# Optimization experiments

Measured on AMD Instinct MI355X. Metric: run time of the kernel, lower is better.

The kernel has to match this reference:

```python
import jax, jax.numpy as jnp
import numpy as np

S, B, E, H = 2048, 2, 1024, 16
D = E // H  # head dim = 64


def setup_inputs() -> dict:
    key = jax.random.key(0)
    k1, k2, k3 = jax.random.split(key, 3)
    x = jax.random.normal(k1, (S, B, E), dtype=jnp.float32)
    Wqkv = jax.random.normal(k2, (3 * E, E), dtype=jnp.float32) * (E ** -0.5)
    bqkv = jax.random.normal(k3, (3 * E,), dtype=jnp.float32) * 0.02
    return {"x": x, "Wqkv": Wqkv, "bqkv": bqkv}


def reference(x, Wqkv, bqkv):
    s, b, e = x.shape
    h, d = H, E // H
    # fused QKV projection: [S,B,E] @ [E,3E] -> [S,B,3E]
    qkv = jnp.einsum('sbe,fe->sbf', x, Wqkv) + bqkv
    q, k, v = jnp.split(qkv, 3, axis=-1)
    q = q.reshape(s, b, h, d)
    k = k.reshape(s, b, h, d)
    v = v.reshape(s, b, h, d)
    scale = 1.0 / jnp.sqrt(jnp.asarray(d, dtype=x.dtype))
    # scores: [B,H,S,S]
    scores = jnp.einsum('sbhd,tbhd->bhst', q, k) * scale
    attn = jax.nn.softmax(scores, axis=-1)
    # context: [S,B,H,D] -> [S,B,E]
    ctx = jnp.einsum('bhst,tbhd->sbhd', attn, v)
    return ctx.reshape(s, b, e)
```

## Files before the change

kernel.cpp:

```cpp
#include <hip/hip_runtime.h>

constexpr int SEQ   = 2048;
constexpr int BATCH = 2;
constexpr int EMB   = 1024;
constexpr int NH    = 16;
constexpr int HDIM  = 64;
constexpr int MROWS = SEQ * BATCH;
constexpr int KDIM  = EMB;
constexpr int NCOLS = 3 * EMB;

typedef __bf16 bf16x8 __attribute__((ext_vector_type(8)));
typedef __bf16 bf16x4 __attribute__((ext_vector_type(4)));
typedef float  f32x4  __attribute__((ext_vector_type(4)));
typedef float  f32x16 __attribute__((ext_vector_type(16)));
typedef unsigned int u32;
typedef unsigned int u32x4 __attribute__((ext_vector_type(4)));

__device__ __forceinline__ u32 cvt_pk_bf16(float lo, float hi) {
  u32 r;
  asm("v_cvt_pk_bf16_f32 %0, %1, %2" : "=v"(r) : "v"(lo), "v"(hi));
  return r;
}
__device__ __forceinline__ void pl32_swap(u32& a, u32& b) {
  asm("v_permlane32_swap_b32 %0, %1" : "+v"(a), "+v"(b));
}
__device__ __forceinline__ void g2l16(const __bf16* g, __bf16* l) {
  __builtin_amdgcn_global_load_lds(
      (const __attribute__((address_space(1))) void*)g,
      (__attribute__((address_space(3))) void*)l, 16, 0, 0);
}

__global__ __launch_bounds__(256) void cvt_f32_bf16(
    const float* __restrict__ src, __bf16* __restrict__ dst, int n4) {
  int stride = gridDim.x * blockDim.x;
  for (int i = blockIdx.x * blockDim.x + threadIdx.x; i < n4; i += stride) {
    float4 v = reinterpret_cast<const float4*>(src)[i];
    bf16x4 o;
    o[0] = (__bf16)v.x; o[1] = (__bf16)v.y; o[2] = (__bf16)v.z; o[3] = (__bf16)v.w;
    reinterpret_cast<bf16x4*>(dst)[i] = o;
  }
}

__global__ __launch_bounds__(256, 4) void qkv_gemm(
    const __bf16* __restrict__ Xb, const __bf16* __restrict__ Wb,
    const float* __restrict__ bqkv,
    __bf16* __restrict__ Qb, __bf16* __restrict__ Kb, __bf16* __restrict__ Vt) {
  __shared__ __attribute__((aligned(16))) __bf16 Al[2][128 * 32];
  __shared__ __attribute__((aligned(16))) __bf16 Bl[2][128 * 32];

  const int tid  = threadIdx.x;
  const int lane = tid & 63;
  const int w    = tid >> 6;
  const int wm   = w >> 1, wn = w & 1;

  const int bid  = blockIdx.x;
  const int wgid = (bid & 7) * 96 + (bid >> 3);
  const int nx   = wgid % 24;
  const int nyy  = wgid / 24;
  const int m0   = nyy * 128;
  const int n0   = nx * 128;

  f32x4 acc[4][4] = {};

  auto stage = [&](int buf, int kt) {
#pragma unroll
    for (int c = 0; c < 2; ++c) {
      const int u   = (w * 2 + c) * 64 + lane;
      const int row = u >> 2;
      const int sc  = ((u & 3) ^ ((row >> 1) & 3)) * 8;
      g2l16(&Xb[(size_t)(m0 + row) * KDIM + kt * 32 + sc], &Al[buf][(w * 2 + c) * 512]);
      g2l16(&Wb[(size_t)(n0 + row) * KDIM + kt * 32 + sc], &Bl[buf][(w * 2 + c) * 512]);
    }
  };

  stage(0, 0);
  __syncthreads();

  const int l15 = lane & 15, hi4 = lane >> 4;
  const int cswz = (hi4 ^ ((l15 >> 1) & 3)) * 8;

  for (int kt = 0; kt < KDIM / 32; ++kt) {
    const int buf = kt & 1;
    if (kt + 1 < KDIM / 32) stage(buf ^ 1, kt + 1);

    bf16x8 af[4], bfr[4];
#pragma unroll
    for (int i = 0; i < 4; ++i) {
      af[i]  = *reinterpret_cast<const bf16x8*>(&Al[buf][(wm * 64 + i * 16 + l15) * 32 + cswz]);
      bfr[i] = *reinterpret_cast<const bf16x8*>(&Bl[buf][(wn * 64 + i * 16 + l15) * 32 + cswz]);
    }
    __builtin_amdgcn_s_setprio(1);
#pragma unroll
    for (int i = 0; i < 4; ++i)
#pragma unroll
      for (int j = 0; j < 4; ++j)
        acc[i][j] = __builtin_amdgcn_mfma_f32_16x16x32_bf16(af[i], bfr[j], acc[i][j], 0, 0, 0);
    __builtin_amdgcn_s_setprio(0);
    __syncthreads();
  }

  const float QSCALE = 0.18033688011112042f;
#pragma unroll
  for (int j = 0; j < 4; ++j) {
    const int f    = n0 + wn * 64 + j * 16 + l15;
    const float bias = bqkv[f];
    const int sec  = f >> 10;
    const int hd   = f & 1023;
    const int h    = hd >> 6, d = hd & 63;
#pragma unroll
    for (int i = 0; i < 4; ++i) {
#pragma unroll
      for (int r = 0; r < 4; ++r) {
        const int mm = m0 + wm * 64 + i * 16 + hi4 * 4 + r;
        const int s_ = mm >> 1, b_ = mm & 1;
        const int bh = b_ * NH + h;
        const float val = acc[i][j][r] + bias;
        if (sec == 0) {
          Qb[((size_t)bh * SEQ + s_) * HDIM + d] = (__bf16)(val * QSCALE);
        } else if (sec == 1) {
          Kb[((size_t)bh * SEQ + s_) * HDIM + d] = (__bf16)val;
        } else {
          Vt[((size_t)bh * HDIM + d) * SEQ + s_] = (__bf16)val;
        }
      }
    }
  }
}

__global__ __launch_bounds__(128, 4) void attn_fwd(
    const __bf16* __restrict__ Qb, const __bf16* __restrict__ Kb,
    const __bf16* __restrict__ Vt, float* __restrict__ out) {
  __shared__ __attribute__((aligned(16))) __bf16 lds[16384];

  const int tid  = threadIdx.x;
  const int lane = tid & 63;
  const int w    = tid >> 6;
  const int lq   = lane & 31;
  const int hi   = lane >> 5;

  const int bid  = blockIdx.x;
  const int wgid = (bid & 7) * 128 + (bid >> 3);
  const int qi   = wgid & 31;
  const int bh   = wgid >> 5;
  const int b_   = bh >> 4, h = bh & 15;
  const int q0   = qi * 64 + w * 32;

  const __bf16* Qp = Qb + (size_t)bh * SEQ * HDIM;
  const __bf16* Kp = Kb + (size_t)bh * SEQ * HDIM;
  const __bf16* Vp = Vt + (size_t)bh * HDIM * SEQ;

  bf16x8 qf[4];
#pragma unroll
  for (int ks = 0; ks < 4; ++ks)
    qf[ks] = *reinterpret_cast<const bf16x8*>(&Qp[(size_t)(q0 + lq) * HDIM + ks * 16 + hi * 8]);

  f32x16 acc0 = {}, acc1 = {};
  float m = -1e30f, l = 0.f;

  auto stage = [&](int b, int t0) {
#pragma unroll
    for (int c = 0; c < 4; ++c) {
      const int u   = (w * 4 + c) * 64 + lane;
      const int row = u >> 3;
      const int sc  = ((u & 7) * 8) ^ ((row & 7) << 3);
      g2l16(Kp + (size_t)(t0 + row) * HDIM + sc, lds + b * 8192 + (w * 4 + c) * 512);
      g2l16(Vp + (size_t)row * SEQ + t0 + sc,    lds + b * 8192 + 4096 + (w * 4 + c) * 512);
    }
  };

  stage(0, 0);
  __syncthreads();

  for (int t0 = 0; t0 < SEQ; t0 += 64) {
    const int cur = (t0 >> 6) & 1;
    if (t0 + 64 < SEQ) stage(cur ^ 1, t0 + 64);
    const __bf16* kb = lds + cur * 8192;
    const __bf16* vb = kb + 4096;

    f32x16 S0 = {}, S1 = {};
    __builtin_amdgcn_s_setprio(1);
#pragma unroll
    for (int ks = 0; ks < 4; ++ks) {
      const int colb = ks * 16 + hi * 8;
      bf16x8 k0 = *reinterpret_cast<const bf16x8*>(&kb[lq * 64        + (colb ^ ((lq & 7) << 3))]);
      bf16x8 k1 = *reinterpret_cast<const bf16x8*>(&kb[(32 + lq) * 64 + (colb ^ ((lq & 7) << 3))]);
      S0 = __builtin_amdgcn_mfma_f32_32x32x16_bf16(k0, qf[ks], S0, 0, 0, 0);
      S1 = __builtin_amdgcn_mfma_f32_32x32x16_bf16(k1, qf[ks], S1, 0, 0, 0);
    }
    __builtin_amdgcn_s_setprio(0);

    float pmax;
    {
      float t0m = fmaxf(S0[0], S0[1]), t1m = fmaxf(S0[2], S0[3]);
      float t2m = fmaxf(S0[4], S0[5]), t3m = fmaxf(S0[6], S0[7]);
      float t4m = fmaxf(S0[8], S0[9]), t5m = fmaxf(S0[10], S0[11]);
      float t6m = fmaxf(S0[12], S0[13]), t7m = fmaxf(S0[14], S0[15]);
      t0m = fmaxf(t0m, t1m); t2m = fmaxf(t2m, t3m); t4m = fmaxf(t4m, t5m); t6m = fmaxf(t6m, t7m);
      float a_ = fmaxf(fmaxf(t0m, t2m), fmaxf(t4m, t6m));
      float u0 = fmaxf(S1[0], S1[1]), u1 = fmaxf(S1[2], S1[3]);
      float u2 = fmaxf(S1[4], S1[5]), u3 = fmaxf(S1[6], S1[7]);
      float u4 = fmaxf(S1[8], S1[9]), u5 = fmaxf(S1[10], S1[11]);
      float u6 = fmaxf(S1[12], S1[13]), u7 = fmaxf(S1[14], S1[15]);
      u0 = fmaxf(u0, u1); u2 = fmaxf(u2, u3); u4 = fmaxf(u4, u5); u6 = fmaxf(u6, u7);
      float b2 = fmaxf(fmaxf(u0, u2), fmaxf(u4, u6));
      pmax = fmaxf(a_, b2);
    }
    pmax = fmaxf(pmax, __shfl_xor(pmax, 32));

    if (__any(pmax > m + 8.f)) {
      const float mnew  = fmaxf(m, pmax);
      const float alpha = __builtin_amdgcn_exp2f(m - mnew);
      m = mnew;
      l *= alpha;
#pragma unroll
      for (int i = 0; i < 16; ++i) { acc0[i] *= alpha; acc1[i] *= alpha; }
    }

    float r0 = 0.f, r1 = 0.f, r2 = 0.f, r3 = 0.f;
#pragma unroll
    for (int i = 0; i < 4; ++i) {
      S0[i]      = __builtin_amdgcn_exp2f(S0[i] - m);      r0 += S0[i];
      S0[i + 4]  = __builtin_amdgcn_exp2f(S0[i + 4] - m);  r1 += S0[i + 4];
      S0[i + 8]  = __builtin_amdgcn_exp2f(S0[i + 8] - m);  r2 += S0[i + 8];
      S0[i + 12] = __builtin_amdgcn_exp2f(S0[i + 12] - m); r3 += S0[i + 12];
    }
#pragma unroll
    for (int i = 0; i < 4; ++i) {
      S1[i]      = __builtin_amdgcn_exp2f(S1[i] - m);      r0 += S1[i];
      S1[i + 4]  = __builtin_amdgcn_exp2f(S1[i + 4] - m);  r1 += S1[i + 4];
      S1[i + 8]  = __builtin_amdgcn_exp2f(S1[i + 8] - m);  r2 += S1[i + 8];
      S1[i + 12] = __builtin_amdgcn_exp2f(S1[i + 12] - m); r3 += S1[i + 12];
    }
    l += (r0 + r1) + (r2 + r3);

    bf16x8 pw[4];
    {
      auto mk = [&](const f32x16& P, bf16x8* dst) {
#pragma unroll
        for (int kk = 0; kk < 2; ++kk) {
          u32 a0 = cvt_pk_bf16(P[kk * 8 + 0], P[kk * 8 + 1]);
          u32 b0 = cvt_pk_bf16(P[kk * 8 + 4], P[kk * 8 + 5]);
          u32 a1 = cvt_pk_bf16(P[kk * 8 + 2], P[kk * 8 + 3]);
          u32 b1 = cvt_pk_bf16(P[kk * 8 + 6], P[kk * 8 + 7]);
          pl32_swap(a0, b0);
          pl32_swap(a1, b1);
          u32x4 wv; wv[0] = a0; wv[1] = a1; wv[2] = b0; wv[3] = b1;
          dst[kk] = __builtin_bit_cast(bf16x8, wv);
        }
      };
      mk(S0, &pw[0]);
      mk(S1, &pw[2]);
    }

    __builtin_amdgcn_s_setprio(1);
#pragma unroll
    for (int ks = 0; ks < 4; ++ks) {
      const int colb = ks * 16 + hi * 8;
      bf16x8 v0 = *reinterpret_cast<const bf16x8*>(&vb[lq * 64        + (colb ^ ((lq & 7) << 3))]);
      bf16x8 v1 = *reinterpret_cast<const bf16x8*>(&vb[(32 + lq) * 64 + (colb ^ ((lq & 7) << 3))]);
      acc0 = __builtin_amdgcn_mfma_f32_32x32x16_bf16(v0, pw[ks], acc0, 0, 0, 0);
      acc1 = __builtin_amdgcn_mfma_f32_32x32x16_bf16(v1, pw[ks], acc1, 0, 0, 0);
    }
    __builtin_amdgcn_s_setprio(0);

    __syncthreads();
  }

  l += __shfl_xor(l, 32);
  const float inv = 1.0f / l;
  const int s_ = q0 + lq;
  float* op = out + ((size_t)s_ * BATCH + b_) * EMB + h * HDIM;
#pragma unroll
  for (int rr = 0; rr < 4; ++rr) {
    float4 o0 = {acc0[4 * rr] * inv, acc0[4 * rr + 1] * inv,
                 acc0[4 * rr + 2] * inv, acc0[4 * rr + 3] * inv};
    *reinterpret_cast<float4*>(&op[8 * rr + 4 * hi]) = o0;
    float4 o1 = {acc1[4 * rr] * inv, acc1[4 * rr + 1] * inv,
                 acc1[4 * rr + 2] * inv, acc1[4 * rr + 3] * inv};
    *reinterpret_cast<float4*>(&op[8 * rr + 4 * hi + 32]) = o1;
  }
}

extern "C" void kernel_launch(void* const* d_in, const int* in_sizes, int n_in,
                              void* d_out, int out_size, void* d_ws, size_t ws_size,
                              hipStream_t stream) {
  (void)in_sizes; (void)n_in; (void)out_size; (void)ws_size;
  const float* x    = (const float*)d_in[0];
  const float* Wqkv = (const float*)d_in[1];
  const float* bias = (const float*)d_in[2];
  float* out = (float*)d_out;

  char* ws = (char*)d_ws;
  __bf16* Xb = (__bf16*)(ws);
  __bf16* Wb = (__bf16*)(ws + 8388608);
  __bf16* Qb = (__bf16*)(ws + 14680064);
  __bf16* Kb = (__bf16*)(ws + 23068672);
  __bf16* Vt = (__bf16*)(ws + 31457280);

  cvt_f32_bf16<<<dim3(1024), dim3(256), 0, stream>>>(x, Xb, (MROWS * KDIM) / 4);
  cvt_f32_bf16<<<dim3(768), dim3(256), 0, stream>>>(Wqkv, Wb, (NCOLS * KDIM) / 4);
  qkv_gemm<<<dim3(768), dim3(256), 0, stream>>>(Xb, Wb, bias, Qb, Kb, Vt);
  attn_fwd<<<dim3(1024), dim3(128), 0, stream>>>(Qb, Kb, Vt, out);
}
```

Baseline: 115.4 us.

## Split attention over key halves with combine kernel; merge conversion launches

Attention is split into two halves of the key sequence (flash-decoding style), doubling the workgroup count to 2048. Each half writes unnormalized partial outputs plus max/sum to workspace, and a new combine kernel merges them. The two fp32-to-bf16 conversion launches are also merged into one. This adds roughly 32 MB of extra partial-output traffic, one more kernel launch, and a dependence on workspace size, with a fallback to the single-pass path when the workspace is too small.

```diff
diff --git a/kernel.cpp b/kernel.cpp
--- a/kernel.cpp
+++ b/kernel.cpp
@@ -30,14 +30,19 @@
       (__attribute__((address_space(3))) void*)l, 16, 0, 0);
 }
 
-__global__ __launch_bounds__(256) void cvt_f32_bf16(
-    const float* __restrict__ src, __bf16* __restrict__ dst, int n4) {
+constexpr int N4X = (MROWS * KDIM) / 4;
+constexpr int N4W = (NCOLS * KDIM) / 4;
+__global__ __launch_bounds__(256) void cvt_all(
+    const float* __restrict__ x, const float* __restrict__ Wq,
+    __bf16* __restrict__ Xb, __bf16* __restrict__ Wb) {
   int stride = gridDim.x * blockDim.x;
-  for (int i = blockIdx.x * blockDim.x + threadIdx.x; i < n4; i += stride) {
-    float4 v = reinterpret_cast<const float4*>(src)[i];
+  for (int i = blockIdx.x * blockDim.x + threadIdx.x; i < N4X + N4W; i += stride) {
+    const float4 v = (i < N4X) ? reinterpret_cast<const float4*>(x)[i]
+                               : reinterpret_cast<const float4*>(Wq)[i - N4X];
     bf16x4 o;
     o[0] = (__bf16)v.x; o[1] = (__bf16)v.y; o[2] = (__bf16)v.z; o[3] = (__bf16)v.w;
-    reinterpret_cast<bf16x4*>(dst)[i] = o;
+    if (i < N4X) reinterpret_cast<bf16x4*>(Xb)[i] = o;
+    else         reinterpret_cast<bf16x4*>(Wb)[i - N4X] = o;
   }
 }
 
@@ -127,9 +132,11 @@
   }
 }
 
+template <int SPLIT>
 __global__ __launch_bounds__(128, 4) void attn_fwd(
     const __bf16* __restrict__ Qb, const __bf16* __restrict__ Kb,
-    const __bf16* __restrict__ Vt, float* __restrict__ out) {
+    const __bf16* __restrict__ Vt, float* __restrict__ out,
+    float* __restrict__ Op, float2* __restrict__ ml) {
   __shared__ __attribute__((aligned(16))) __bf16 lds[16384];
 
   const int tid  = threadIdx.x;
@@ -138,12 +145,19 @@
   const int lq   = lane & 31;
   const int hi   = lane >> 5;
 
-  const int bid  = blockIdx.x;
-  const int wgid = (bid & 7) * 128 + (bid >> 3);
-  const int qi   = wgid & 31;
-  const int bh   = wgid >> 5;
-  const int b_   = bh >> 4, h = bh & 15;
-  const int q0   = qi * 64 + w * 32;
+  const int bid = blockIdx.x;
+  int bh, qi, half, t_begin, nt;
+  if constexpr (SPLIT) {
+    const int wgid = (bid & 7) * 256 + (bid >> 3);
+    bh = wgid >> 6; qi = (wgid >> 1) & 31; half = wgid & 1;
+    t_begin = half * (SEQ / 2); nt = SEQ / 128;
+  } else {
+    const int wgid = (bid & 7) * 128 + (bid >> 3);
+    bh = wgid >> 5; qi = wgid & 31; half = 0;
+    t_begin = 0; nt = SEQ / 64;
+  }
+  const int b_ = bh >> 4, h = bh & 15;
+  const int q0 = qi * 64 + w * 32;
 
   const __bf16* Qp = Qb + (size_t)bh * SEQ * HDIM;
   const __bf16* Kp = Kb + (size_t)bh * SEQ * HDIM;
@@ -168,12 +182,12 @@
     }
   };
 
-  stage(0, 0);
+  stage(0, t_begin);
   __syncthreads();
 
-  for (int t0 = 0; t0 < SEQ; t0 += 64) {
-    const int cur = (t0 >> 6) & 1;
-    if (t0 + 64 < SEQ) stage(cur ^ 1, t0 + 64);
+  for (int it = 0; it < nt; ++it) {
+    const int cur = it & 1;
+    if (it + 1 < nt) stage(cur ^ 1, t_begin + (it + 1) * 64);
     const __bf16* kb = lds + cur * 8192;
     const __bf16* vb = kb + 4096;
 
@@ -267,24 +281,58 @@
   }
 
   l += __shfl_xor(l, 32);
-  const float inv = 1.0f / l;
-  const int s_ = q0 + lq;
-  float* op = out + ((size_t)s_ * BATCH + b_) * EMB + h * HDIM;
-#pragma unroll
-  for (int rr = 0; rr < 4; ++rr) {
-    float4 o0 = {acc0[4 * rr] * inv, acc0[4 * rr + 1] * inv,
-                 acc0[4 * rr + 2] * inv, acc0[4 * rr + 3] * inv};
-    *reinterpret_cast<float4*>(&op[8 * rr + 4 * hi]) = o0;
-    float4 o1 = {acc1[4 * rr] * inv, acc1[4 * rr + 1] * inv,
-                 acc1[4 * rr + 2] * inv, acc1[4 * rr + 3] * inv};
-    *reinterpret_cast<float4*>(&op[8 * rr + 4 * hi + 32]) = o1;
-  }
+  if constexpr (SPLIT) {
+    const int rowg = (bh * 32 + qi) * 64 + w * 32 + lq;
+    float* pp = Op + ((size_t)rowg * 2 + half) * 64;
+#pragma unroll
+    for (int rr = 0; rr < 4; ++rr) {
+      float4 o0 = {acc0[4 * rr], acc0[4 * rr + 1], acc0[4 * rr + 2], acc0[4 * rr + 3]};
+      *reinterpret_cast<float4*>(&pp[8 * rr + 4 * hi]) = o0;
+      float4 o1 = {acc1[4 * rr], acc1[4 * rr + 1], acc1[4 * rr + 2], acc1[4 * rr + 3]};
+      *reinterpret_cast<float4*>(&pp[8 * rr + 4 * hi + 32]) = o1;
+    }
+    if (hi == 0) ml[rowg * 2 + half] = make_float2(m, l);
+  } else {
+    const float inv = 1.0f / l;
+    const int s_ = q0 + lq;
+    float* op = out + ((size_t)s_ * BATCH + b_) * EMB + h * HDIM;
+#pragma unroll
+    for (int rr = 0; rr < 4; ++rr) {
+      float4 o0 = {acc0[4 * rr] * inv, acc0[4 * rr + 1] * inv,
+                   acc0[4 * rr + 2] * inv, acc0[4 * rr + 3] * inv};
+      *reinterpret_cast<float4*>(&op[8 * rr + 4 * hi]) = o0;
+      float4 o1 = {acc1[4 * rr] * inv, acc1[4 * rr + 1] * inv,
+                   acc1[4 * rr + 2] * inv, acc1[4 * rr + 3] * inv};
+      *reinterpret_cast<float4*>(&op[8 * rr + 4 * hi + 32]) = o1;
+    }
+  }
+}
+
+__global__ __launch_bounds__(256) void attn_combine(
+    const float* __restrict__ Op, const float2* __restrict__ ml,
+    float* __restrict__ out) {
+  const int idx  = blockIdx.x * 256 + threadIdx.x;
+  const int rowg = idx >> 4;
+  const int c    = idx & 15;
+  const float2 a = ml[rowg * 2];
+  const float2 b = ml[rowg * 2 + 1];
+  const float M  = fmaxf(a.x, b.x);
+  const float w0 = __builtin_amdgcn_exp2f(a.x - M);
+  const float w1 = __builtin_amdgcn_exp2f(b.x - M);
+  const float inv = 1.0f / (a.y * w0 + b.y * w1);
+  const float4 o0 = *reinterpret_cast<const float4*>(&Op[((size_t)rowg * 2) * 64 + c * 4]);
+  const float4 o1 = *reinterpret_cast<const float4*>(&Op[((size_t)rowg * 2 + 1) * 64 + c * 4]);
+  float4 o = {(o0.x * w0 + o1.x * w1) * inv, (o0.y * w0 + o1.y * w1) * inv,
+              (o0.z * w0 + o1.z * w1) * inv, (o0.w * w0 + o1.w * w1) * inv};
+  const int bh = rowg >> 11, s_ = rowg & 2047;
+  const int b_ = bh >> 4, h = bh & 15;
+  *reinterpret_cast<float4*>(&out[((size_t)s_ * BATCH + b_) * EMB + h * HDIM + c * 4]) = o;
 }
 
 extern "C" void kernel_launch(void* const* d_in, const int* in_sizes, int n_in,
                               void* d_out, int out_size, void* d_ws, size_t ws_size,
                               hipStream_t stream) {
-  (void)in_sizes; (void)n_in; (void)out_size; (void)ws_size;
+  (void)in_sizes; (void)n_in; (void)out_size;
   const float* x    = (const float*)d_in[0];
   const float* Wqkv = (const float*)d_in[1];
   const float* bias = (const float*)d_in[2];
@@ -296,9 +344,16 @@
   __bf16* Qb = (__bf16*)(ws + 14680064);
   __bf16* Kb = (__bf16*)(ws + 23068672);
   __bf16* Vt = (__bf16*)(ws + 31457280);
-
-  cvt_f32_bf16<<<dim3(1024), dim3(256), 0, stream>>>(x, Xb, (MROWS * KDIM) / 4);
-  cvt_f32_bf16<<<dim3(768), dim3(256), 0, stream>>>(Wqkv, Wb, (NCOLS * KDIM) / 4);
+  float*  Op = (float*)(ws + 39845888);
+  float2* ml = (float2*)(ws + 73400320);
+  const size_t NEED = 74448896;
+
+  cvt_all<<<dim3(2048), dim3(256), 0, stream>>>(x, Wqkv, Xb, Wb);
   qkv_gemm<<<dim3(768), dim3(256), 0, stream>>>(Xb, Wb, bias, Qb, Kb, Vt);
-  attn_fwd<<<dim3(1024), dim3(128), 0, stream>>>(Qb, Kb, Vt, out);
-}
+  if (ws_size >= NEED) {
+    attn_fwd<1><<<dim3(2048), dim3(128), 0, stream>>>(Qb, Kb, Vt, out, Op, ml);
+    attn_combine<<<dim3(4096), dim3(256), 0, stream>>>(Op, ml, out);
+  } else {
+    attn_fwd<0><<<dim3(1024), dim3(128), 0, stream>>>(Qb, Kb, Vt, out, Op, ml);
+  }
+}
```

Result: slower. 123.3 us (+6.9%).
